# Kernel tuning notes

Hardware: AMD Instinct MI355X
Metric: run time of the kernel (lower is better)

Reference implementation:

```python
import jax, jax.numpy as jnp
import numpy as np

N_ELEMENTS = 1_000_000
D_FEAT = 128
N_SEGMENTS = 16384


def setup_inputs() -> dict:
    key = jax.random.key(0)
    kx, ki = jax.random.split(key)
    x = jax.random.normal(kx, (N_ELEMENTS, D_FEAT), dtype=jnp.float32)
    index = jnp.sort(jax.random.randint(ki, (N_ELEMENTS,), 0, N_SEGMENTS, dtype=jnp.int64))
    return {"x": x, "index": index}


def reference(x, index):
    # scatter_add(x, index, dim=0): out[s] = sum over rows i with index[i] == s
    return jax.ops.segment_sum(x, index, num_segments=N_SEGMENTS)
```

## Files before the change

kernel.cpp:

```cpp
#include <hip/hip_runtime.h>
#include <hip/hip_bf16.h>


constexpr int D_FEAT = 128;
constexpr int D2 = D_FEAT / 2;
constexpr int ROWS_PER_WAVE = 128;
constexpr int WAVES_PER_BLOCK = 4;

__global__ void zero_out_kernel(float4* __restrict__ out, int n4) {
    int i = blockIdx.x * blockDim.x + threadIdx.x;
    int stride = gridDim.x * blockDim.x;
    for (; i < n4; i += stride) {
        out[i] = make_float4(0.f, 0.f, 0.f, 0.f);
    }
}

__global__ __launch_bounds__(256) void segsum_kernel(
        const float* __restrict__ x,
        const int* __restrict__ index,
        float* __restrict__ out,
        int n_rows) {
    const int wave_in_block = threadIdx.x >> 6;
    const int lane = threadIdx.x & 63;
    const long wave = (long)blockIdx.x * WAVES_PER_BLOCK + wave_in_block;

    long row0 = wave * ROWS_PER_WAVE;
    if (row0 >= n_rows) return;
    long rend = row0 + ROWS_PER_WAVE;
    if (rend > n_rows) rend = n_rows;

    const float2* __restrict__ x2 = (const float2*)x;

    float2 acc = make_float2(0.f, 0.f);
    int cur_seg = index[row0];

    for (long r = row0; r < rend; ++r) {
        int s = index[r];
        float2 v = x2[r * D2 + lane];
        if (s != cur_seg) {
            float* o = out + (long)cur_seg * D_FEAT + 2 * lane;
            atomicAdd(o, acc.x);
            atomicAdd(o + 1, acc.y);
            cur_seg = s;
            acc = v;
        } else {
            acc.x += v.x;
            acc.y += v.y;
        }
    }
    float* o = out + (long)cur_seg * D_FEAT + 2 * lane;
    atomicAdd(o, acc.x);
    atomicAdd(o + 1, acc.y);
}

extern "C" void kernel_launch(void* const* d_in, const int* in_sizes, int n_in,
                              void* d_out, int out_size, void* d_ws, size_t ws_size,
                              hipStream_t stream) {
    const float* x = (const float*)d_in[0];
    const int* index = (const int*)d_in[1];
    float* out = (float*)d_out;

    const int n_rows = in_sizes[1];
    const int n_out4 = out_size / 4;

    zero_out_kernel<<<256, 256, 0, stream>>>((float4*)out, n_out4);

    const long n_waves = ((long)n_rows + ROWS_PER_WAVE - 1) / ROWS_PER_WAVE;
    const int n_blocks = (int)((n_waves + WAVES_PER_BLOCK - 1) / WAVES_PER_BLOCK);
    segsum_kernel<<<n_blocks, 256, 0, stream>>>(x, index, out, n_rows);
}
```

Measured before the change: 669.0 us.

## Use float4 half-wave row split with unrolled, software-prefetched segmented accumulation

Each wave now splits into two 32-lane halves, and each half handles alternate rows with float4 loads, so one wave covers two rows per load. The main loop processes 8 rows per iteration with int4 index loads, prefetches the next iteration's data into registers, and takes a fast path when all four of a lane's rows share one segment. The aim is more memory parallelism and fewer dependent load-add chains in a bandwidth-bound loop. In exchange the code is more complex and uses more registers, and each half-wave flushes its own partial sum, which doubles the atomics at segment boundaries. The zero-fill grid is also doubled.

```diff
diff --git a/kernel.cpp b/kernel.cpp
--- a/kernel.cpp
+++ b/kernel.cpp
@@ -3,7 +3,7 @@
 
 
 constexpr int D_FEAT = 128;
-constexpr int D2 = D_FEAT / 2;
+constexpr int D4 = D_FEAT / 4;
 constexpr int ROWS_PER_WAVE = 128;
 constexpr int WAVES_PER_BLOCK = 4;
 
@@ -22,6 +22,8 @@
         int n_rows) {
     const int wave_in_block = threadIdx.x >> 6;
     const int lane = threadIdx.x & 63;
+    const int half = lane >> 5;
+    const int sub = lane & 31;
     const long wave = (long)blockIdx.x * WAVES_PER_BLOCK + wave_in_block;
 
     long row0 = wave * ROWS_PER_WAVE;
@@ -29,28 +31,76 @@
     long rend = row0 + ROWS_PER_WAVE;
     if (rend > n_rows) rend = n_rows;
 
-    const float2* __restrict__ x2 = (const float2*)x;
+    const float4* __restrict__ x4 = (const float4*)x;
 
-    float2 acc = make_float2(0.f, 0.f);
-    int cur_seg = index[row0];
+    float4 acc = make_float4(0.f, 0.f, 0.f, 0.f);
+    long myrow0 = row0 + half;
+    int cur_seg = index[myrow0 < rend ? myrow0 : (rend - 1)];
 
-    for (long r = row0; r < rend; ++r) {
-        int s = index[r];
-        float2 v = x2[r * D2 + lane];
+    auto flush = [&]() {
+        float* o = out + (long)cur_seg * D_FEAT + (sub << 2);
+        atomicAdd(o + 0, acc.x);
+        atomicAdd(o + 1, acc.y);
+        atomicAdd(o + 2, acc.z);
+        atomicAdd(o + 3, acc.w);
+    };
+    auto step1 = [&](int s, const float4& v) {
         if (s != cur_seg) {
-            float* o = out + (long)cur_seg * D_FEAT + 2 * lane;
-            atomicAdd(o, acc.x);
-            atomicAdd(o + 1, acc.y);
+            flush();
             cur_seg = s;
             acc = v;
         } else {
-            acc.x += v.x;
-            acc.y += v.y;
+            acc.x += v.x; acc.y += v.y; acc.z += v.z; acc.w += v.w;
+        }
+    };
+
+    const long nmain = (rend - row0) >> 3;
+
+    const float4* p = x4 + (row0 + half) * D4 + sub;
+    const int* ip = index + row0;
+
+    float4 va0 = acc, va1 = acc, va2 = acc, va3 = acc;
+    float4 vb0 = acc, vb1 = acc, vb2 = acc, vb3 = acc;
+    int4 ia = make_int4(0, 0, 0, 0), ib = ia, ja = ia, jb = ia;
+
+    if (nmain > 0) {
+        ia = *(const int4*)(ip);
+        ib = *(const int4*)(ip + 4);
+        va0 = p[0]; va1 = p[64]; va2 = p[128]; va3 = p[192];
+    }
+    for (long t = 0; t < nmain; ++t) {
+        if (t + 1 < nmain) {
+            ja = *(const int4*)(ip + 8);
+            jb = *(const int4*)(ip + 12);
+            const float4* pn = p + 256;
+            vb0 = pn[0]; vb1 = pn[64]; vb2 = pn[128]; vb3 = pn[192];
+        }
+        int s0 = half ? ia.y : ia.x;
+        int s1 = half ? ia.w : ia.z;
+        int s2 = half ? ib.y : ib.x;
+        int s3 = half ? ib.w : ib.z;
+        if (s0 == cur_seg && s3 == cur_seg) {
+            acc.x += (va0.x + va1.x) + (va2.x + va3.x);
+            acc.y += (va0.y + va1.y) + (va2.y + va3.y);
+            acc.z += (va0.z + va1.z) + (va2.z + va3.z);
+            acc.w += (va0.w + va1.w) + (va2.w + va3.w);
+        } else {
+            step1(s0, va0); step1(s1, va1); step1(s2, va2); step1(s3, va3);
+        }
+        ia = ja; ib = jb;
+        va0 = vb0; va1 = vb1; va2 = vb2; va3 = vb3;
+        p += 256; ip += 8;
+    }
+
+    for (long r = row0 + nmain * 8; r < rend; r += 2) {
+        long my_r = r + half;
+        if (my_r < rend) {
+            int s = index[my_r];
+            float4 v = x4[my_r * D4 + sub];
+            step1(s, v);
         }
     }
-    float* o = out + (long)cur_seg * D_FEAT + 2 * lane;
-    atomicAdd(o, acc.x);
-    atomicAdd(o + 1, acc.y);
+    flush();
 }
 
 extern "C" void kernel_launch(void* const* d_in, const int* in_sizes, int n_in,
@@ -63,7 +113,7 @@
     const int n_rows = in_sizes[1];
     const int n_out4 = out_size / 4;
 
-    zero_out_kernel<<<256, 256, 0, stream>>>((float4*)out, n_out4);
+    zero_out_kernel<<<512, 256, 0, stream>>>((float4*)out, n_out4);
 
     const long n_waves = ((long)n_rows + ROWS_PER_WAVE - 1) / ROWS_PER_WAVE;
     const int n_blocks = (int)((n_waves + WAVES_PER_BLOCK - 1) / WAVES_PER_BLOCK);
```

Result: no change. 669.9 us (+0.1%).
